# Optimization experiments

Measured on AMD Instinct MI355X. Metric: run time of the kernel, lower is better.

The kernel has to match this reference:

```python
import jax, jax.numpy as jnp
import numpy as np

NUM_CLASSES = 80
ANCHORS = np.array([[10,13],[16,30],[33,23],[30,61],[62,45],[59,119],[116,90],[156,198],[373,326]], np.float32)
MASK = [[0,1,2],[3,4,5],[6,7,8]]
STRIDES = [8, 16, 32]
MAX_OUT = 100      # max_output_size_per_class == max_total_size
IOU_THR = 0.45
SCORE_THR = 0.25
NMS_TOPK = 128     # per-class candidate pre-selection for greedy NMS (>= MAX_OUT)


def setup_inputs() -> dict:
    key = jax.random.key(0)
    k1, k2, k3 = jax.random.split(key, 3)
    B = 16
    C = 3 * (NUM_CLASSES + 5)  # 255
    return {
        'p3': jax.random.normal(k1, (B, 80, 80, C), jnp.float32),
        'p4': jax.random.normal(k2, (B, 40, 40, C), jnp.float32),
        'p5': jax.random.normal(k3, (B, 20, 20, C), jnp.float32),
    }


def _decode(logits, anchors, stride):
    # logits: [B,H,W,3*(nc+5)] -> boxes [B,H*W*3,4] (x1y1x2y2), obj [B,M], cls [B,M,nc]
    B, H, W, _ = logits.shape
    A = anchors.shape[0]
    x = logits.reshape(B, H, W, A, NUM_CLASSES + 5)
    xy = jax.nn.sigmoid(x[..., :2])
    wh_logit = x[..., 2:4]
    obj = jax.nn.sigmoid(x[..., 4])
    cls = jax.nn.sigmoid(x[..., 5:])
    gx, gy = jnp.meshgrid(jnp.arange(W, dtype=x.dtype), jnp.arange(H, dtype=x.dtype))
    grid = jnp.stack([gx, gy], axis=-1)[:, :, None, :]  # [H,W,1,2]
    ctr = (xy + grid) * stride
    wh = jnp.exp(wh_logit) * anchors  # [B,H,W,A,2]
    box = jnp.concatenate([ctr - wh / 2.0, ctr + wh / 2.0], axis=-1)
    return box.reshape(B, -1, 4), obj.reshape(B, -1), cls.reshape(B, -1, NUM_CLASSES)


def _pairwise_iou(b):
    # b: [K,4] x1y1x2y2 -> [K,K]
    area = (b[:, 2] - b[:, 0]) * (b[:, 3] - b[:, 1])
    lt = jnp.maximum(b[:, None, :2], b[None, :, :2])
    rb = jnp.minimum(b[:, None, 2:], b[None, :, 2:])
    wh = jnp.clip(rb - lt, 0.0)
    inter = wh[..., 0] * wh[..., 1]
    return inter / (area[:, None] + area[None, :] - inter + 1e-9)


def _nms_single(boxes, scores):
    # boxes [N,4], scores [N] for one (image, class): greedy NMS on top-K candidates
    s = jnp.where(scores > SCORE_THR, scores, -1.0)
    top_s, idx = jax.lax.top_k(s, NMS_TOPK)   # sorted descending
    b = boxes[idx]                            # [K,4]
    iou = _pairwise_iou(b)                    # [K,K]
    rng = jnp.arange(NMS_TOPK)

    def body(keep, i):
        active = keep[i] & (top_s[i] > 0.0)
        sup = active & (iou[i] > IOU_THR) & (rng > i)
        return keep & ~sup, None

    keep, _ = jax.lax.scan(body, jnp.ones(NMS_TOPK, bool), rng)
    valid = keep & (top_s > 0.0)
    ss = jnp.where(valid, top_s, -1.0)
    sel_s, sel_i = jax.lax.top_k(ss, MAX_OUT)
    return b[sel_i], sel_s                    # [M,4], [M]


def _per_image(boxes, scores_cn):
    # boxes [N,4] shared across classes (q=1), scores_cn [C,N]
    cb, cs = jax.vmap(_nms_single, in_axes=(None, 0))(boxes, scores_cn)  # [C,M,4],[C,M]
    C = cs.shape[0]
    cls_id = jnp.broadcast_to(jnp.arange(C, dtype=boxes.dtype)[:, None], cs.shape)
    fs, fi = jax.lax.top_k(cs.reshape(-1), MAX_OUT)
    fb = cb.reshape(-1, 4)[fi]
    fc = cls_id.reshape(-1)[fi]
    valid = fs > 0.0
    n_valid = jnp.sum(valid).astype(jnp.int32)
    return (jnp.where(valid[:, None], fb, 0.0),
            jnp.where(valid, fs, 0.0),
            jnp.where(valid, fc, 0.0),
            n_valid)


def _forward(p3, p4, p5):
    boxes, objs, clss = [], [], []
    for logits, m, stride in zip((p3, p4, p5), MASK, STRIDES):
        b, o, c = _decode(logits, jnp.asarray(ANCHORS[m]), float(stride))
        boxes.append(b); objs.append(o); clss.append(c)
    boxes = jnp.concatenate(boxes, axis=1)   # [B,N,4]
    obj = jnp.concatenate(objs, axis=1)      # [B,N]
    cls = jnp.concatenate(clss, axis=1)      # [B,N,C]
    scores = obj[..., None] * cls            # [B,N,C]
    return jax.vmap(_per_image)(boxes, scores.transpose(0, 2, 1))


def reference(p3, p4, p5):
    # returns (boxes [B,100,4], scores [B,100], classes [B,100], valid [B])
    return _forward(p3, p4, p5)
```

## Files before the change

### kernel.cpp

```cpp
#include <hip/hip_runtime.h>
#include <stdint.h>

#define NUM_CLASSES 80
#define N_ANCH 25200
#define B_IMG 16
#define NMS_TOPK_ 128
#define MAX_OUT_ 100
#define SCORE_THR_ 0.25f
#define IOU_THR_ 0.45f
#define NBINS 2048
#define CAP 2048
#define CAPB 512
#define CAPC 256

__constant__ float c_anch[9][2] = {
    {10.f, 13.f}, {16.f, 30.f}, {33.f, 23.f},
    {30.f, 61.f}, {62.f, 45.f}, {59.f, 119.f},
    {116.f, 90.f}, {156.f, 198.f}, {373.f, 326.f}};

__device__ __forceinline__ float sigmoidf_(float x) {
    return 1.0f / (1.0f + expf(-x));
}

__device__ __forceinline__ unsigned int score_bin(unsigned int bits) {
    unsigned int bin = (bits - 0x3E800000u) >> 13;
    if (bin >= NBINS) bin = NBINS - 1;
    return bin;
}


__global__ void __launch_bounds__(256) decode_scores_kernel(
    const float* __restrict__ p3, const float* __restrict__ p4,
    const float* __restrict__ p5, float* __restrict__ boxes,
    float* __restrict__ score_t) {
    int blk = blockIdx.x;
    int b = blk / 525;
    int tile = blk - b * 525;
    const float* p; int W, lvl, il0, base;
    if (tile < 400)      { p = p3; W = 80; lvl = 0; il0 = tile * 48;         base = 0;     }
    else if (tile < 500) { p = p4; W = 40; lvl = 1; il0 = (tile - 400) * 48; base = 19200; }
    else                 { p = p5; W = 20; lvl = 2; il0 = (tile - 500) * 48; base = 24000; }
    float stride = (float)(8 << lvl);
    const float* src = p + (size_t)b * ((size_t)W * W * 255) + (size_t)il0 * 85;

    __shared__ float raw[48 * 85];
    __shared__ float obj_sh[48];
    int tid = threadIdx.x;

    for (int k = tid; k < 48 * 85; k += 256) raw[k] = src[k];
    __syncthreads();

    if (tid < 48) {
        int il = il0 + tid;
        int y = il / (W * 3);
        int t = il - y * (W * 3);
        int x = t / 3;
        int a = t - x * 3;
        const float* q = &raw[tid * 85];
        float cx = (sigmoidf_(q[0]) + (float)x) * stride;
        float cy = (sigmoidf_(q[1]) + (float)y) * stride;
        float bw = expf(q[2]) * c_anch[lvl * 3 + a][0];
        float bh = expf(q[3]) * c_anch[lvl * 3 + a][1];
        int gi = base + il;
        float* bo = boxes + ((size_t)b * N_ANCH + gi) * 4;
        bo[0] = cx - bw * 0.5f; bo[1] = cy - bh * 0.5f;
        bo[2] = cx + bw * 0.5f; bo[3] = cy + bh * 0.5f;
        obj_sh[tid] = sigmoidf_(q[4]);
    }
    __syncthreads();

    int gi0 = base + il0;
    for (int o = tid; o < NUM_CLASSES * 48; o += 256) {
        int c = o / 48;
        int j = o - c * 48;
        float s = obj_sh[j] * sigmoidf_(raw[j * 85 + 5 + c]);
        score_t[((size_t)(b * NUM_CLASSES + c)) * N_ANCH + gi0 + j] = s;
    }
}

__global__ void __launch_bounds__(256) topk_nms_fast_kernel(
    const float* __restrict__ score_t, const float* __restrict__ boxes,
    float* __restrict__ cls_score, float* __restrict__ cls_box) {
    int b = blockIdx.x / NUM_CLASSES;
    int c = blockIdx.x % NUM_CLASSES;
    int tid = threadIdx.x;
    const float* sc = score_t + (size_t)(b * NUM_CLASSES + c) * N_ANCH;
    const float4* sc4 = (const float4*)sc;

    __shared__ unsigned int hist[NBINS];
    __shared__ unsigned int segsum[256];
    __shared__ unsigned long long keys[CAPB];
    __shared__ unsigned int s_cnt;
    __shared__ int s_cut;
    __shared__ float bx[NMS_TOPK_][5];
    __shared__ float bs[NMS_TOPK_];
    __shared__ int keep[NMS_TOPK_];

    for (int k = tid; k < NBINS; k += 256) hist[k] = 0u;
    if (tid == 0) s_cnt = 0u;
    __syncthreads();

    for (int i = tid; i < N_ANCH / 4; i += 256) {
        float4 v = sc4[i];
        float vv[4] = {v.x, v.y, v.z, v.w};
#pragma unroll
        for (int k = 0; k < 4; ++k) {
            if (vv[k] > SCORE_THR_)
                atomicAdd(&hist[score_bin(__float_as_uint(vv[k]))], 1u);
        }
    }
    __syncthreads();

    unsigned int ss = 0;
    for (int k = 0; k < 8; ++k) ss += hist[tid * 8 + k];
    segsum[tid] = ss;
    __syncthreads();
    if (tid == 0) {
        unsigned int tot = 0; int cut = 0; int t = 255;
        for (; t >= 0; --t) {
            if (tot + segsum[t] >= NMS_TOPK_) break;
            tot += segsum[t];
        }
        if (t >= 0) {
            int j = 7;
            for (; j >= 0; --j) { tot += hist[t * 8 + j]; if (tot >= NMS_TOPK_) break; }
            if (j < 0) j = 0;
            cut = t * 8 + j;
        }
        s_cut = cut;
    }
    __syncthreads();
    unsigned int cutoff = (unsigned int)s_cut;

    for (int i = tid; i < N_ANCH / 4; i += 256) {
        float4 v = sc4[i];
        float vv[4] = {v.x, v.y, v.z, v.w};
#pragma unroll
        for (int k = 0; k < 4; ++k) {
            if (vv[k] > SCORE_THR_) {
                unsigned int bits = __float_as_uint(vv[k]);
                if (score_bin(bits) >= cutoff) {
                    unsigned int pos = atomicAdd(&s_cnt, 1u);
                    if (pos < CAPB) {
                        keys[pos] = ((unsigned long long)bits << 32) |
                                    (unsigned long long)(~(unsigned int)(i * 4 + k));
                    }
                }
            }
        }
    }
    __syncthreads();

    unsigned int M = s_cnt;
    if (M > CAPB) M = CAPB;
    unsigned int P2 = 1;
    while (P2 < M) P2 <<= 1;
    if (P2 < 2) P2 = 2;
    for (unsigned int k = M + tid; k < P2; k += 256) keys[k] = 0ull;
    __syncthreads();

    for (unsigned int k = 2; k <= P2; k <<= 1) {
        for (unsigned int j = k >> 1; j > 0; j >>= 1) {
            for (unsigned int t = tid; t < P2; t += 256) {
                unsigned int ixj = t ^ j;
                if (ixj > t) {
                    unsigned long long a0 = keys[t], b0 = keys[ixj];
                    bool desc = ((t & k) == 0);
                    if (desc ? (a0 < b0) : (a0 > b0)) { keys[t] = b0; keys[ixj] = a0; }
                }
            }
            __syncthreads();
        }
    }

    unsigned int K = M < NMS_TOPK_ ? M : NMS_TOPK_;
    if (tid < (int)K) {
        unsigned long long kk = keys[tid];
        unsigned int idx = ~((unsigned int)(kk & 0xFFFFFFFFull));
        const float* bp = boxes + ((size_t)b * N_ANCH + idx) * 4;
        bx[tid][0] = bp[0]; bx[tid][1] = bp[1];
        bx[tid][2] = bp[2]; bx[tid][3] = bp[3];
        bs[tid] = __uint_as_float((unsigned int)(kk >> 32));
        keep[tid] = 1;
    }
    __syncthreads();

    for (unsigned int i = 0; i < K; ++i) {
        if (keep[i]) {
            unsigned int t = (unsigned int)tid;
            if (t > i && t < K && keep[t]) {
                float ax0 = bx[i][0], ay0 = bx[i][1], ax1 = bx[i][2], ay1 = bx[i][3];
                float cx0 = bx[t][0], cy0 = bx[t][1], cx1 = bx[t][2], cy1 = bx[t][3];
                float areaA = (ax1 - ax0) * (ay1 - ay0);
                float areaB = (cx1 - cx0) * (cy1 - cy0);
                float lx = fmaxf(ax0, cx0), ly = fmaxf(ay0, cy0);
                float rx = fminf(ax1, cx1), ry = fminf(ay1, cy1);
                float w = rx - lx; if (w < 0.f) w = 0.f;
                float h = ry - ly; if (h < 0.f) h = 0.f;
                float inter = w * h;
                float iou = inter / (areaA + areaB - inter + 1e-9f);
                if (iou > IOU_THR_) keep[t] = 0;
            }
        }
        __syncthreads();
    }

    if (tid == 0) {
        float* scd = cls_score + ((size_t)b * NUM_CLASSES + c) * MAX_OUT_;
        float* bod = cls_box + ((size_t)b * NUM_CLASSES + c) * MAX_OUT_ * 4;
        int out_n = 0;
        for (unsigned int t2 = 0; t2 < K && out_n < MAX_OUT_; ++t2) {
            if (keep[t2]) {
                scd[out_n] = bs[t2];
                bod[out_n * 4 + 0] = bx[t2][0];
                bod[out_n * 4 + 1] = bx[t2][1];
                bod[out_n * 4 + 2] = bx[t2][2];
                bod[out_n * 4 + 3] = bx[t2][3];
                out_n++;
            }
        }
        for (; out_n < MAX_OUT_; ++out_n) {
            scd[out_n] = -1.0f;
            bod[out_n * 4 + 0] = 0.f; bod[out_n * 4 + 1] = 0.f;
            bod[out_n * 4 + 2] = 0.f; bod[out_n * 4 + 3] = 0.f;
        }
    }
}

__global__ void __launch_bounds__(256) final_fast_kernel(
    const float* __restrict__ cls_score, const float* __restrict__ cls_box,
    float* __restrict__ out) {
    int b = blockIdx.x;
    int tid = threadIdx.x;
    const int NC = NUM_CLASSES * MAX_OUT_;
    const float* sc = cls_score + (size_t)b * NC;

    __shared__ unsigned int hist[NBINS];
    __shared__ unsigned int segsum[256];
    __shared__ unsigned long long keys[CAPC];
    __shared__ unsigned int s_cnt, s_tot;
    __shared__ int s_cut;

    for (int k = tid; k < NBINS; k += 256) hist[k] = 0u;
    if (tid == 0) s_cnt = 0u;
    __syncthreads();

    for (int k = tid; k < NC; k += 256) {
        float s = sc[k];
        if (s > 0.0f) atomicAdd(&hist[score_bin(__float_as_uint(s))], 1u);
    }
    __syncthreads();

    unsigned int ss = 0;
    for (int k = 0; k < 8; ++k) ss += hist[tid * 8 + k];
    segsum[tid] = ss;
    __syncthreads();
    if (tid == 0) {
        unsigned int total = 0;
        for (int t = 0; t < 256; ++t) total += segsum[t];
        s_tot = total;
        unsigned int tot = 0; int cut = 0; int t = 255;
        for (; t >= 0; --t) {
            if (tot + segsum[t] >= MAX_OUT_) break;
            tot += segsum[t];
        }
        if (t >= 0) {
            int j = 7;
            for (; j >= 0; --j) { tot += hist[t * 8 + j]; if (tot >= MAX_OUT_) break; }
            if (j < 0) j = 0;
            cut = t * 8 + j;
        }
        s_cut = cut;
    }
    __syncthreads();
    unsigned int cutoff = (unsigned int)s_cut;

    for (int k = tid; k < NC; k += 256) {
        float s = sc[k];
        if (s > 0.0f && score_bin(__float_as_uint(s)) >= cutoff) {
            unsigned int pos = atomicAdd(&s_cnt, 1u);
            if (pos < CAPC) {
                keys[pos] = ((unsigned long long)__float_as_uint(s) << 32) |
                            (unsigned long long)(~(unsigned int)k);
            }
        }
    }
    __syncthreads();

    unsigned int M = s_cnt;
    if (M > CAPC) M = CAPC;
    unsigned int P2 = 1;
    while (P2 < M) P2 <<= 1;
    if (P2 < 2) P2 = 2;
    for (unsigned int k = M + tid; k < P2; k += 256) keys[k] = 0ull;
    __syncthreads();

    for (unsigned int k = 2; k <= P2; k <<= 1) {
        for (unsigned int j = k >> 1; j > 0; j >>= 1) {
            for (unsigned int t = tid; t < P2; t += 256) {
                unsigned int ixj = t ^ j;
                if (ixj > t) {
                    unsigned long long a0 = keys[t], b0 = keys[ixj];
                    bool desc = ((t & k) == 0);
                    if (desc ? (a0 < b0) : (a0 > b0)) { keys[t] = b0; keys[ixj] = a0; }
                }
            }
            __syncthreads();
        }
    }

    float* ob = out;
    float* os = out + B_IMG * MAX_OUT_ * 4;
    float* oc = os + B_IMG * MAX_OUT_;
    float* on = oc + B_IMG * MAX_OUT_;

    unsigned int K = M < MAX_OUT_ ? M : MAX_OUT_;
    if (tid < MAX_OUT_) {
        if ((unsigned int)tid < K) {
            unsigned long long kk = keys[tid];
            unsigned int flat = ~((unsigned int)(kk & 0xFFFFFFFFull));
            float sv = __uint_as_float((unsigned int)(kk >> 32));
            const float* bp = cls_box + ((size_t)b * NC + flat) * 4;
            os[b * MAX_OUT_ + tid] = sv;
            oc[b * MAX_OUT_ + tid] = (float)(flat / MAX_OUT_);
            ob[(b * MAX_OUT_ + tid) * 4 + 0] = bp[0];
            ob[(b * MAX_OUT_ + tid) * 4 + 1] = bp[1];
            ob[(b * MAX_OUT_ + tid) * 4 + 2] = bp[2];
            ob[(b * MAX_OUT_ + tid) * 4 + 3] = bp[3];
        } else {
            os[b * MAX_OUT_ + tid] = 0.0f;
            oc[b * MAX_OUT_ + tid] = 0.0f;
            ob[(b * MAX_OUT_ + tid) * 4 + 0] = 0.0f;
            ob[(b * MAX_OUT_ + tid) * 4 + 1] = 0.0f;
            ob[(b * MAX_OUT_ + tid) * 4 + 2] = 0.0f;
            ob[(b * MAX_OUT_ + tid) * 4 + 3] = 0.0f;
        }
    }
    if (tid == 0) {
        unsigned int nv = s_tot < MAX_OUT_ ? s_tot : MAX_OUT_;
        on[b] = (float)nv;
    }
}


__global__ void __launch_bounds__(256) decode_kernel(
    const float* __restrict__ p3, const float* __restrict__ p4,
    const float* __restrict__ p5, float* __restrict__ boxes,
    float* __restrict__ obj) {
    int gid = blockIdx.x * blockDim.x + threadIdx.x;
    if (gid >= B_IMG * N_ANCH) return;
    int b = gid / N_ANCH;
    int i = gid - b * N_ANCH;
    const float* p; int W, il, lvl; float stride;
    if (i < 19200)      { p = p3; W = 80; il = i;         lvl = 0; stride = 8.f;  }
    else if (i < 24000) { p = p4; W = 40; il = i - 19200; lvl = 1; stride = 16.f; }
    else                { p = p5; W = 20; il = i - 24000; lvl = 2; stride = 32.f; }
    int y = il / (W * 3);
    int t = il - y * W * 3;
    int x = t / 3;
    int a = t - x * 3;
    const float* q = p + ((((size_t)b * W + y) * W + x) * 255 + a * 85);
    float cx = (sigmoidf_(q[0]) + (float)x) * stride;
    float cy = (sigmoidf_(q[1]) + (float)y) * stride;
    float bw = expf(q[2]) * c_anch[lvl * 3 + a][0];
    float bh = expf(q[3]) * c_anch[lvl * 3 + a][1];
    float* bo = boxes + (size_t)gid * 4;
    bo[0] = cx - bw * 0.5f; bo[1] = cy - bh * 0.5f;
    bo[2] = cx + bw * 0.5f; bo[3] = cy + bh * 0.5f;
    obj[gid] = sigmoidf_(q[4]);
}

__device__ __forceinline__ float cand_score(
    const float* __restrict__ p3, const float* __restrict__ p4,
    const float* __restrict__ p5, const float* __restrict__ obj,
    int b, int c, int i) {
    const float* p; int W, il;
    if (i < 19200)      { p = p3; W = 80; il = i;         }
    else if (i < 24000) { p = p4; W = 40; il = i - 19200; }
    else                { p = p5; W = 20; il = i - 24000; }
    int y = il / (W * 3);
    int t = il - y * W * 3;
    int x = t / 3;
    int a = t - x * 3;
    float cl = p[(((size_t)b * W + y) * W + x) * 255 + a * 85 + 5 + c];
    return obj[b * N_ANCH + i] * sigmoidf_(cl);
}

__global__ void __launch_bounds__(256) topk_nms_kernel(
    const float* __restrict__ p3, const float* __restrict__ p4,
    const float* __restrict__ p5, const float* __restrict__ boxes,
    const float* __restrict__ obj, float* __restrict__ cls_score,
    float* __restrict__ cls_box) {
    int b = blockIdx.x / NUM_CLASSES;
    int c = blockIdx.x % NUM_CLASSES;
    int tid = threadIdx.x;

    __shared__ unsigned int hist[NBINS];
    __shared__ unsigned long long keys[CAP];
    __shared__ unsigned int s_cnt, s_cutoff;
    __shared__ float bx[NMS_TOPK_][5];
    __shared__ float bs[NMS_TOPK_];
    __shared__ int keep[NMS_TOPK_];

    for (int k = tid; k < NBINS; k += 256) hist[k] = 0u;
    if (tid == 0) s_cnt = 0u;
    __syncthreads();

    for (int i = tid; i < N_ANCH; i += 256) {
        float s = cand_score(p3, p4, p5, obj, b, c, i);
        if (s > SCORE_THR_) atomicAdd(&hist[score_bin(__float_as_uint(s))], 1u);
    }
    __syncthreads();

    if (tid == 0) {
        unsigned int total = 0;
        int cut = 0;
        for (int k = NBINS - 1; k >= 0; --k) {
            total += hist[k];
            if (total >= NMS_TOPK_) { cut = k; break; }
        }
        s_cutoff = (unsigned int)cut;
    }
    __syncthreads();
    unsigned int cutoff = s_cutoff;

    for (int i = tid; i < N_ANCH; i += 256) {
        float s = cand_score(p3, p4, p5, obj, b, c, i);
        if (s > SCORE_THR_) {
            unsigned int bits = __float_as_uint(s);
            if (score_bin(bits) >= cutoff) {
                unsigned int pos = atomicAdd(&s_cnt, 1u);
                if (pos < CAP) {
                    keys[pos] = ((unsigned long long)bits << 32) |
                                (unsigned long long)(~(unsigned int)i);
                }
            }
        }
    }
    __syncthreads();

    unsigned int M = s_cnt;
    if (M > CAP) M = CAP;
    unsigned int P2 = 1;
    while (P2 < M) P2 <<= 1;
    if (P2 < 2) P2 = 2;
    for (unsigned int k = M + tid; k < P2; k += 256) keys[k] = 0ull;
    __syncthreads();

    for (unsigned int k = 2; k <= P2; k <<= 1) {
        for (unsigned int j = k >> 1; j > 0; j >>= 1) {
            for (unsigned int t = tid; t < P2; t += 256) {
                unsigned int ixj = t ^ j;
                if (ixj > t) {
                    unsigned long long a0 = keys[t], b0 = keys[ixj];
                    bool desc = ((t & k) == 0);
                    if (desc ? (a0 < b0) : (a0 > b0)) { keys[t] = b0; keys[ixj] = a0; }
                }
            }
            __syncthreads();
        }
    }

    unsigned int K = M < NMS_TOPK_ ? M : NMS_TOPK_;
    if (tid < (int)K) {
        unsigned long long kk = keys[tid];
        unsigned int idx = ~((unsigned int)(kk & 0xFFFFFFFFull));
        const float* bp = boxes + ((size_t)b * N_ANCH + idx) * 4;
        bx[tid][0] = bp[0]; bx[tid][1] = bp[1];
        bx[tid][2] = bp[2]; bx[tid][3] = bp[3];
        bs[tid] = __uint_as_float((unsigned int)(kk >> 32));
        keep[tid] = 1;
    }
    __syncthreads();

    for (unsigned int i = 0; i < K; ++i) {
        if (keep[i]) {
            unsigned int t = (unsigned int)tid;
            if (t > i && t < K && keep[t]) {
                float ax0 = bx[i][0], ay0 = bx[i][1], ax1 = bx[i][2], ay1 = bx[i][3];
                float cx0 = bx[t][0], cy0 = bx[t][1], cx1 = bx[t][2], cy1 = bx[t][3];
                float areaA = (ax1 - ax0) * (ay1 - ay0);
                float areaB = (cx1 - cx0) * (cy1 - cy0);
                float lx = fmaxf(ax0, cx0), ly = fmaxf(ay0, cy0);
                float rx = fminf(ax1, cx1), ry = fminf(ay1, cy1);
                float w = rx - lx; if (w < 0.f) w = 0.f;
                float h = ry - ly; if (h < 0.f) h = 0.f;
                float inter = w * h;
                float iou = inter / (areaA + areaB - inter + 1e-9f);
                if (iou > IOU_THR_) keep[t] = 0;
            }
        }
        __syncthreads();
    }

    if (tid == 0) {
        float* scd = cls_score + ((size_t)b * NUM_CLASSES + c) * MAX_OUT_;
        float* bod = cls_box + ((size_t)b * NUM_CLASSES + c) * MAX_OUT_ * 4;
        int out_n = 0;
        for (unsigned int t2 = 0; t2 < K && out_n < MAX_OUT_; ++t2) {
            if (keep[t2]) {
                scd[out_n] = bs[t2];
                bod[out_n * 4 + 0] = bx[t2][0];
                bod[out_n * 4 + 1] = bx[t2][1];
                bod[out_n * 4 + 2] = bx[t2][2];
                bod[out_n * 4 + 3] = bx[t2][3];
                out_n++;
            }
        }
        for (; out_n < MAX_OUT_; ++out_n) {
            scd[out_n] = -1.0f;
            bod[out_n * 4 + 0] = 0.f; bod[out_n * 4 + 1] = 0.f;
            bod[out_n * 4 + 2] = 0.f; bod[out_n * 4 + 3] = 0.f;
        }
    }
}

extern "C" void kernel_launch(void* const* d_in, const int* in_sizes, int n_in,
                              void* d_out, int out_size, void* d_ws, size_t ws_size,
                              hipStream_t stream) {
    const float* p3 = (const float*)d_in[0];
    const float* p4 = (const float*)d_in[1];
    const float* p5 = (const float*)d_in[2];

    const size_t score_t_elems = (size_t)B_IMG * NUM_CLASSES * N_ANCH;
    const size_t boxes_elems   = (size_t)B_IMG * N_ANCH * 4;
    const size_t clsS_elems    = (size_t)B_IMG * NUM_CLASSES * MAX_OUT_;
    const size_t clsB_elems    = clsS_elems * 4;
    const size_t need_fast = (score_t_elems + boxes_elems + clsS_elems + clsB_elems) * sizeof(float);

    float* ws = (float*)d_ws;

    if (ws_size >= need_fast) {
        float* score_t  = ws;
        float* boxes    = score_t + score_t_elems;
        float* cls_score = boxes + boxes_elems;
        float* cls_box  = cls_score + clsS_elems;

        decode_scores_kernel<<<B_IMG * 525, 256, 0, stream>>>(p3, p4, p5, boxes, score_t);
        topk_nms_fast_kernel<<<B_IMG * NUM_CLASSES, 256, 0, stream>>>(
            score_t, boxes, cls_score, cls_box);
        final_fast_kernel<<<B_IMG, 256, 0, stream>>>(cls_score, cls_box, (float*)d_out);
    } else {
        float* boxes = ws;
        float* obj = boxes + boxes_elems;
        float* cls_score = obj + (size_t)B_IMG * N_ANCH;
        float* cls_box = cls_score + clsS_elems;

        int tot = B_IMG * N_ANCH;
        decode_kernel<<<(tot + 255) / 256, 256, 0, stream>>>(p3, p4, p5, boxes, obj);
        topk_nms_kernel<<<B_IMG * NUM_CLASSES, 256, 0, stream>>>(
            p3, p4, p5, boxes, obj, cls_score, cls_box);
        final_fast_kernel<<<B_IMG, 256, 0, stream>>>(cls_score, cls_box, (float*)d_out);
    }
}
```

Baseline: 348.8 us.

## Vectorize decode I/O and move bitonic sort and greedy NMS into one wavefront

The decode kernel now works on 80-anchor tiles, loads raw logits as float4 and writes the transposed class scores as float4 vectors. The per-class top-k kernel runs its bitonic sort in a single 64-lane wavefront, which removes the block-wide barrier after every sort stage. Greedy NMS now runs in one wavefront with keep flags held in registers and ballot masks instead of a shared array and a barrier per candidate. Output compaction uses popcount prefix positions rather than a serial loop on thread 0. The cost is less parallelism in the sort, with three of the four waves idle, and the single-wave sort depends on lockstep wavefront execution plus block-level fences for correctness.

Result: faster. 336.5 us (-3.5%).

```diff
diff --git a/kernel.cpp b/kernel.cpp
--- a/kernel.cpp
+++ b/kernel.cpp
@@ -12,6 +12,7 @@
 #define CAP 2048
 #define CAPB 512
 #define CAPC 256
+#define TILE_A 80
 
 __constant__ float c_anch[9][2] = {
     {10.f, 13.f}, {16.f, 30.f}, {33.f, 23.f},
@@ -34,23 +35,25 @@
     const float* __restrict__ p5, float* __restrict__ boxes,
     float* __restrict__ score_t) {
     int blk = blockIdx.x;
-    int b = blk / 525;
-    int tile = blk - b * 525;
+    int b = blk / 315;
+    int tile = blk - b * 315;
     const float* p; int W, lvl, il0, base;
-    if (tile < 400)      { p = p3; W = 80; lvl = 0; il0 = tile * 48;         base = 0;     }
-    else if (tile < 500) { p = p4; W = 40; lvl = 1; il0 = (tile - 400) * 48; base = 19200; }
-    else                 { p = p5; W = 20; lvl = 2; il0 = (tile - 500) * 48; base = 24000; }
+    if (tile < 240)      { p = p3; W = 80; lvl = 0; il0 = tile * TILE_A;         base = 0;     }
+    else if (tile < 300) { p = p4; W = 40; lvl = 1; il0 = (tile - 240) * TILE_A; base = 19200; }
+    else                 { p = p5; W = 20; lvl = 2; il0 = (tile - 300) * TILE_A; base = 24000; }
     float stride = (float)(8 << lvl);
-    const float* src = p + (size_t)b * ((size_t)W * W * 255) + (size_t)il0 * 85;
-
-    __shared__ float raw[48 * 85];
-    __shared__ float obj_sh[48];
+
+    __shared__ float4 raw4[TILE_A * 85 / 4];
+    __shared__ float obj_sh[TILE_A];
+    float* raw = (float*)raw4;
     int tid = threadIdx.x;
 
-    for (int k = tid; k < 48 * 85; k += 256) raw[k] = src[k];
-    __syncthreads();
-
-    if (tid < 48) {
+    const float4* src4 = (const float4*)(p + (size_t)b * ((size_t)W * W * 255) +
+                                         (size_t)il0 * 85);
+    for (int k = tid; k < TILE_A * 85 / 4; k += 256) raw4[k] = src4[k];
+    __syncthreads();
+
+    if (tid < TILE_A) {
         int il = il0 + tid;
         int y = il / (W * 3);
         int t = il - y * (W * 3);
@@ -70,11 +73,17 @@
     __syncthreads();
 
     int gi0 = base + il0;
-    for (int o = tid; o < NUM_CLASSES * 48; o += 256) {
-        int c = o / 48;
-        int j = o - c * 48;
-        float s = obj_sh[j] * sigmoidf_(raw[j * 85 + 5 + c]);
-        score_t[((size_t)(b * NUM_CLASSES + c)) * N_ANCH + gi0 + j] = s;
+    for (int o = tid; o < NUM_CLASSES * (TILE_A / 4); o += 256) {
+        int c = o / (TILE_A / 4);
+        int q = o - c * (TILE_A / 4);
+        int j = q * 4;
+        float4 v;
+        v.x = obj_sh[j + 0] * sigmoidf_(raw[(j + 0) * 85 + 5 + c]);
+        v.y = obj_sh[j + 1] * sigmoidf_(raw[(j + 1) * 85 + 5 + c]);
+        v.z = obj_sh[j + 2] * sigmoidf_(raw[(j + 2) * 85 + 5 + c]);
+        v.w = obj_sh[j + 3] * sigmoidf_(raw[(j + 3) * 85 + 5 + c]);
+        float4* dst = (float4*)(score_t + ((size_t)(b * NUM_CLASSES + c)) * N_ANCH + gi0);
+        dst[q] = v;
     }
 }
 
@@ -84,17 +93,16 @@
     int b = blockIdx.x / NUM_CLASSES;
     int c = blockIdx.x % NUM_CLASSES;
     int tid = threadIdx.x;
-    const float* sc = score_t + (size_t)(b * NUM_CLASSES + c) * N_ANCH;
-    const float4* sc4 = (const float4*)sc;
+    int lane = tid & 63;
+    int wave = tid >> 6;
+    const float4* sc4 = (const float4*)(score_t + (size_t)(b * NUM_CLASSES + c) * N_ANCH);
 
     __shared__ unsigned int hist[NBINS];
     __shared__ unsigned int segsum[256];
-    __shared__ unsigned long long keys[CAPB];
+    __shared__ unsigned long long sel[CAPB];
+    __shared__ float bx[NMS_TOPK_][5];
     __shared__ unsigned int s_cnt;
     __shared__ int s_cut;
-    __shared__ float bx[NMS_TOPK_][5];
-    __shared__ float bs[NMS_TOPK_];
-    __shared__ int keep[NMS_TOPK_];
 
     for (int k = tid; k < NBINS; k += 256) hist[k] = 0u;
     if (tid == 0) s_cnt = 0u;
@@ -142,8 +150,8 @@
                 if (score_bin(bits) >= cutoff) {
                     unsigned int pos = atomicAdd(&s_cnt, 1u);
                     if (pos < CAPB) {
-                        keys[pos] = ((unsigned long long)bits << 32) |
-                                    (unsigned long long)(~(unsigned int)(i * 4 + k));
+                        sel[pos] = ((unsigned long long)bits << 32) |
+                                   (unsigned long long)(~(unsigned int)(i * 4 + k));
                     }
                 }
             }
@@ -156,73 +164,104 @@
     unsigned int P2 = 1;
     while (P2 < M) P2 <<= 1;
     if (P2 < 2) P2 = 2;
-    for (unsigned int k = M + tid; k < P2; k += 256) keys[k] = 0ull;
-    __syncthreads();
-
-    for (unsigned int k = 2; k <= P2; k <<= 1) {
-        for (unsigned int j = k >> 1; j > 0; j >>= 1) {
-            for (unsigned int t = tid; t < P2; t += 256) {
-                unsigned int ixj = t ^ j;
-                if (ixj > t) {
-                    unsigned long long a0 = keys[t], b0 = keys[ixj];
-                    bool desc = ((t & k) == 0);
-                    if (desc ? (a0 < b0) : (a0 > b0)) { keys[t] = b0; keys[ixj] = a0; }
-                }
-            }
-            __syncthreads();
-        }
-    }
+    for (unsigned int k = M + tid; k < P2; k += 256) sel[k] = 0ull;
+    __syncthreads();
+
+    if (wave == 0) {
+        for (unsigned int k = 2; k <= P2; k <<= 1) {
+            for (unsigned int j = k >> 1; j > 0; j >>= 1) {
+                for (unsigned int t = (unsigned int)lane; t < P2; t += 64) {
+                    unsigned int ixj = t ^ j;
+                    if (ixj > t) {
+                        unsigned long long a0 = sel[t], b0 = sel[ixj];
+                        bool desc = ((t & k) == 0);
+                        if (desc ? (a0 < b0) : (a0 > b0)) { sel[t] = b0; sel[ixj] = a0; }
+                    }
+                }
+                __threadfence_block();
+            }
+        }
+    }
+    __syncthreads();
 
     unsigned int K = M < NMS_TOPK_ ? M : NMS_TOPK_;
     if (tid < (int)K) {
-        unsigned long long kk = keys[tid];
+        unsigned long long kk = sel[tid];
         unsigned int idx = ~((unsigned int)(kk & 0xFFFFFFFFull));
         const float* bp = boxes + ((size_t)b * N_ANCH + idx) * 4;
         bx[tid][0] = bp[0]; bx[tid][1] = bp[1];
         bx[tid][2] = bp[2]; bx[tid][3] = bp[3];
-        bs[tid] = __uint_as_float((unsigned int)(kk >> 32));
-        keep[tid] = 1;
-    }
-    __syncthreads();
-
-    for (unsigned int i = 0; i < K; ++i) {
-        if (keep[i]) {
-            unsigned int t = (unsigned int)tid;
-            if (t > i && t < K && keep[t]) {
-                float ax0 = bx[i][0], ay0 = bx[i][1], ax1 = bx[i][2], ay1 = bx[i][3];
-                float cx0 = bx[t][0], cy0 = bx[t][1], cx1 = bx[t][2], cy1 = bx[t][3];
-                float areaA = (ax1 - ax0) * (ay1 - ay0);
-                float areaB = (cx1 - cx0) * (cy1 - cy0);
-                float lx = fmaxf(ax0, cx0), ly = fmaxf(ay0, cy0);
-                float rx = fminf(ax1, cx1), ry = fminf(ay1, cy1);
-                float w = rx - lx; if (w < 0.f) w = 0.f;
-                float h = ry - ly; if (h < 0.f) h = 0.f;
-                float inter = w * h;
-                float iou = inter / (areaA + areaB - inter + 1e-9f);
-                if (iou > IOU_THR_) keep[t] = 0;
-            }
-        }
-        __syncthreads();
-    }
-
-    if (tid == 0) {
+        bx[tid][4] = __uint_as_float((unsigned int)(kk >> 32));
+    }
+    __syncthreads();
+
+    if (wave == 0) {
+        bool k0 = (unsigned int)lane < K;
+        bool k1 = (unsigned int)(64 + lane) < K;
+        float x00 = 0, y00 = 0, x01 = 0, y01 = 0, a0 = 0, sv0 = 0;
+        float x10 = 0, y10 = 0, x11 = 0, y11 = 0, a1 = 0, sv1 = 0;
+        if (k0) {
+            x00 = bx[lane][0]; y00 = bx[lane][1];
+            x01 = bx[lane][2]; y01 = bx[lane][3]; sv0 = bx[lane][4];
+            a0 = (x01 - x00) * (y01 - y00);
+        }
+        if (k1) {
+            x10 = bx[64 + lane][0]; y10 = bx[64 + lane][1];
+            x11 = bx[64 + lane][2]; y11 = bx[64 + lane][3]; sv1 = bx[64 + lane][4];
+            a1 = (x11 - x10) * (y11 - y10);
+        }
+        unsigned long long km0 = __ballot(k0);
+        unsigned long long km1 = __ballot(k1);
+        for (unsigned int i = 0; i < K; ++i) {
+            bool ki = ((((i < 64) ? km0 : km1) >> (i & 63)) & 1ull) != 0ull;
+            if (ki) {
+                float rx0 = bx[i][0], ry0 = bx[i][1], rx1 = bx[i][2], ry1 = bx[i][3];
+                float ra = (rx1 - rx0) * (ry1 - ry0);
+                if (k0 && (unsigned int)lane > i) {
+                    float lx = fmaxf(rx0, x00), ly = fmaxf(ry0, y00);
+                    float rx = fminf(rx1, x01), ry = fminf(ry1, y01);
+                    float w = fmaxf(rx - lx, 0.f), h = fmaxf(ry - ly, 0.f);
+                    float inter = w * h;
+                    float iou = inter / (ra + a0 - inter + 1e-9f);
+                    if (iou > IOU_THR_) k0 = false;
+                }
+                if (k1 && (unsigned int)(64 + lane) > i) {
+                    float lx = fmaxf(rx0, x10), ly = fmaxf(ry0, y10);
+                    float rx = fminf(rx1, x11), ry = fminf(ry1, y11);
+                    float w = fmaxf(rx - lx, 0.f), h = fmaxf(ry - ly, 0.f);
+                    float inter = w * h;
+                    float iou = inter / (ra + a1 - inter + 1e-9f);
+                    if (iou > IOU_THR_) k1 = false;
+                }
+                km0 = __ballot(k0);
+                km1 = __ballot(k1);
+            }
+        }
         float* scd = cls_score + ((size_t)b * NUM_CLASSES + c) * MAX_OUT_;
-        float* bod = cls_box + ((size_t)b * NUM_CLASSES + c) * MAX_OUT_ * 4;
-        int out_n = 0;
-        for (unsigned int t2 = 0; t2 < K && out_n < MAX_OUT_; ++t2) {
-            if (keep[t2]) {
-                scd[out_n] = bs[t2];
-                bod[out_n * 4 + 0] = bx[t2][0];
-                bod[out_n * 4 + 1] = bx[t2][1];
-                bod[out_n * 4 + 2] = bx[t2][2];
-                bod[out_n * 4 + 3] = bx[t2][3];
-                out_n++;
-            }
-        }
-        for (; out_n < MAX_OUT_; ++out_n) {
-            scd[out_n] = -1.0f;
-            bod[out_n * 4 + 0] = 0.f; bod[out_n * 4 + 1] = 0.f;
-            bod[out_n * 4 + 2] = 0.f; bod[out_n * 4 + 3] = 0.f;
+        float* bod = cls_box + ((size_t)b * NUM_CLASSES + c) * (MAX_OUT_ * 4);
+        int n0 = __popcll(km0);
+        int n = n0 + __popcll(km1);
+        if (k0) {
+            int pos = __popcll(km0 & ((1ull << lane) - 1ull));
+            if (pos < MAX_OUT_) {
+                scd[pos] = sv0;
+                bod[pos * 4 + 0] = x00; bod[pos * 4 + 1] = y00;
+                bod[pos * 4 + 2] = x01; bod[pos * 4 + 3] = y01;
+            }
+        }
+        if (k1) {
+            int pos = n0 + __popcll(km1 & ((1ull << lane) - 1ull));
+            if (pos < MAX_OUT_) {
+                scd[pos] = sv1;
+                bod[pos * 4 + 0] = x10; bod[pos * 4 + 1] = y10;
+                bod[pos * 4 + 2] = x11; bod[pos * 4 + 3] = y11;
+            }
+        }
+        int start = n < MAX_OUT_ ? n : MAX_OUT_;
+        for (int p2 = start + lane; p2 < MAX_OUT_; p2 += 64) {
+            scd[p2] = -1.0f;
+            bod[p2 * 4 + 0] = 0.f; bod[p2 * 4 + 1] = 0.f;
+            bod[p2 * 4 + 2] = 0.f; bod[p2 * 4 + 3] = 0.f;
         }
     }
 }
@@ -295,19 +334,22 @@
     for (unsigned int k = M + tid; k < P2; k += 256) keys[k] = 0ull;
     __syncthreads();
 
-    for (unsigned int k = 2; k <= P2; k <<= 1) {
-        for (unsigned int j = k >> 1; j > 0; j >>= 1) {
-            for (unsigned int t = tid; t < P2; t += 256) {
-                unsigned int ixj = t ^ j;
-                if (ixj > t) {
-                    unsigned long long a0 = keys[t], b0 = keys[ixj];
-                    bool desc = ((t & k) == 0);
-                    if (desc ? (a0 < b0) : (a0 > b0)) { keys[t] = b0; keys[ixj] = a0; }
-                }
-            }
-            __syncthreads();
-        }
-    }
+    if (tid < 64) {
+        for (unsigned int k = 2; k <= P2; k <<= 1) {
+            for (unsigned int j = k >> 1; j > 0; j >>= 1) {
+                for (unsigned int t = (unsigned int)tid; t < P2; t += 64) {
+                    unsigned int ixj = t ^ j;
+                    if (ixj > t) {
+                        unsigned long long a0 = keys[t], b0 = keys[ixj];
+                        bool desc = ((t & k) == 0);
+                        if (desc ? (a0 < b0) : (a0 > b0)) { keys[t] = b0; keys[ixj] = a0; }
+                    }
+                }
+                __threadfence_block();
+            }
+        }
+    }
+    __syncthreads();
 
     float* ob = out;
     float* os = out + B_IMG * MAX_OUT_ * 4;
@@ -531,12 +573,12 @@
     float* ws = (float*)d_ws;
 
     if (ws_size >= need_fast) {
-        float* score_t  = ws;
-        float* boxes    = score_t + score_t_elems;
+        float* score_t   = ws;
+        float* boxes     = score_t + score_t_elems;
         float* cls_score = boxes + boxes_elems;
-        float* cls_box  = cls_score + clsS_elems;
-
-        decode_scores_kernel<<<B_IMG * 525, 256, 0, stream>>>(p3, p4, p5, boxes, score_t);
+        float* cls_box   = cls_score + clsS_elems;
+
+        decode_scores_kernel<<<B_IMG * 315, 256, 0, stream>>>(p3, p4, p5, boxes, score_t);
         topk_nms_fast_kernel<<<B_IMG * NUM_CLASSES, 256, 0, stream>>>(
             score_t, boxes, cls_score, cls_box);
         final_fast_kernel<<<B_IMG, 256, 0, stream>>>(cls_score, cls_box, (float*)d_out);
```
